# Kernel optimization log

Hardware: AMD Instinct MI355X
Metric: run time of the kernel (lower is better)

The kernel has to match this reference:

```python
import jax, jax.numpy as jnp
import numpy as np

N_NODES = 100000
N_EDGES = 1000000
N_GRAPHS = 2048
MOL_DIM = 9
HID = 64


def setup_inputs() -> dict:
    key = jax.random.key(0)
    ks = jax.random.split(key, 16)
    x = jax.random.normal(ks[0], (N_NODES, MOL_DIM), dtype=jnp.float32)
    edge_src = jax.random.randint(ks[1], (N_EDGES,), 0, N_NODES)
    edge_dst = jax.random.randint(ks[2], (N_EDGES,), 0, N_NODES)
    batch = jnp.sort(jax.random.randint(ks[3], (N_NODES,), 0, N_GRAPHS))
    def lin(k, fan_in, fan_out):
        bound = 1.0 / np.sqrt(fan_in)
        kw, kb = jax.random.split(k)
        W = jax.random.uniform(kw, (fan_in, fan_out), minval=-bound, maxval=bound, dtype=jnp.float32)
        b = jax.random.uniform(kb, (fan_out,), minval=-bound, maxval=bound, dtype=jnp.float32)
        return W, b
    W1, b1 = lin(ks[4], MOL_DIM, HID)
    W2, b2 = lin(ks[5], HID, HID)
    W3, b3 = lin(ks[6], HID, HID)
    Wp1, bp1 = lin(ks[7], 2 * HID, 64)
    Wp2, bp2 = lin(ks[8], 64, 1)
    return dict(x=x, edge_src=edge_src, edge_dst=edge_dst, batch=batch,
                W1=W1, b1=b1, W2=W2, b2=b2, W3=W3, b3=b3,
                Wp1=Wp1, bp1=bp1, Wp2=Wp2, bp2=bp2)


def gcn_conv(x, edge_src, edge_dst, W, b):
    # PyG GCNConv: add self-loops, symmetric D^-1/2 (A+I) D^-1/2 normalization.
    n = x.shape[0]
    h = x @ W  # [N, out]
    ones = jnp.ones_like(edge_dst, dtype=h.dtype)
    deg = jax.ops.segment_sum(ones, edge_dst, num_segments=n) + 1.0  # self-loop counted
    dinv = jax.lax.rsqrt(deg)
    norm = dinv[edge_src] * dinv[edge_dst]  # [E]
    msg = h[edge_src] * norm[:, None]       # gather + scale
    agg = jax.ops.segment_sum(msg, edge_dst, num_segments=n)
    agg = agg + h * (1.0 / deg)[:, None]    # self-loop contribution (norm = 1/deg)
    return agg + b


def reference(x, edge_src, edge_dst, batch, W1, b1, W2, b2, W3, b3, Wp1, bp1, Wp2, bp2):
    h = jax.nn.relu(gcn_conv(x, edge_src, edge_dst, W1, b1))
    h = jax.nn.relu(gcn_conv(h, edge_src, edge_dst, W2, b2))
    h = jax.nn.relu(gcn_conv(h, edge_src, edge_dst, W3, b3))
    # global mean / max pool by graph id
    counts = jax.ops.segment_sum(jnp.ones((h.shape[0],), h.dtype), batch, num_segments=N_GRAPHS)
    sums = jax.ops.segment_sum(h, batch, num_segments=N_GRAPHS)
    mean = sums / jnp.maximum(counts, 1.0)[:, None]
    mx = jax.ops.segment_max(h, batch, num_segments=N_GRAPHS)
    mx = jnp.where(counts[:, None] > 0, mx, 0.0)
    g = jnp.concatenate([mean, mx], axis=1)  # [G, 128]
    # predictor (dropout inactive in eval mode)
    out = jax.nn.relu(g @ Wp1 + bp1) @ Wp2 + bp2
    return out
```

## Files before the change

kernel.cpp:

```cpp
#include <hip/hip_runtime.h>

#define NN 100000
#define NE 1000000
#define NG 2048
#define NBLK 98
#define CSRCAP 1800000

__device__ __forceinline__ float rl(float v, int k) {
    return __int_as_float(__builtin_amdgcn_readlane(__float_as_int(v), k));
}
__device__ __forceinline__ int rfl(int v) { return __builtin_amdgcn_readfirstlane(v); }

#define PDEG(c) (((c) + 7) & ~7)


__global__ void k_cnt(const int* __restrict__ dst, int* __restrict__ cnt,
                      int* __restrict__ ticket,
                      const int* __restrict__ batch, int* __restrict__ pcnt) {
    int i = blockIdx.x * blockDim.x + threadIdx.x;
    if (i < NE) ticket[i] = atomicAdd(&cnt[dst[i]], 1);
    if (i < NN) atomicAdd(&pcnt[batch[i]], 1);
}

__global__ void k_scan1(const int* __restrict__ cnt, int* __restrict__ bsum,
                        const float* __restrict__ x, float* __restrict__ dinv,
                        float* __restrict__ px, float* __restrict__ p1,
                        float* __restrict__ p2) {
    int t = threadIdx.x;
    int base = blockIdx.x * 1024 + t * 4;
    int4 v = {0, 0, 0, 0};
    if (base < NN) v = *(const int4*)(cnt + base);
    int s = PDEG(v.x) + PDEG(v.y) + PDEG(v.z) + PDEG(v.w);
    #pragma unroll
    for (int off = 32; off; off >>= 1) s += __shfl_down(s, off, 64);
    __shared__ int ws[4];
    if ((t & 63) == 0) ws[t >> 6] = s;
    __syncthreads();
    if (t == 0) bsum[blockIdx.x] = ws[0] + ws[1] + ws[2] + ws[3];

    if (base < NN) {
        int c[4] = {v.x, v.y, v.z, v.w};
        #pragma unroll
        for (int j2 = 0; j2 < 4; ++j2) {
            int nd = base + j2;
            float dv = rsqrtf((float)(c[j2] + 1));
            dinv[nd] = dv;
            #pragma unroll
            for (int j = 0; j < 9; ++j) px[nd * 9 + j] = x[nd * 9 + j] * dv;
        }
    } else if (base == NN) {
        #pragma unroll
        for (int j = 0; j < 9; ++j) px[NN * 9 + j] = 0.f;
        for (int j = 0; j < 64; ++j) {
            p1[(size_t)NN * 64 + j] = 0.f;
            p2[(size_t)NN * 64 + j] = 0.f;
        }
    }
}

__global__ void k_scan2(const int* __restrict__ bsum, int* __restrict__ boff, int nb) {
    __shared__ int buf[128];
    int t = threadIdx.x;
    int v = (t < nb) ? bsum[t] : 0;
    buf[t] = v;
    __syncthreads();
    for (int off = 1; off < 128; off <<= 1) {
        int u = (t >= off) ? buf[t - off] : 0;
        __syncthreads();
        buf[t] += u;
        __syncthreads();
    }
    if (t < nb) boff[t] = buf[t] - v;
}

__global__ void k_scan3(const int* __restrict__ cnt, const int* __restrict__ boff,
                        int* __restrict__ prp, int n) {
    int t = threadIdx.x;
    int base = blockIdx.x * 1024 + t * 4;
    int4 v = {0, 0, 0, 0};
    if (base < n) v = *(const int4*)(cnt + base);
    int p0 = PDEG(v.x), p1 = PDEG(v.y), p2 = PDEG(v.z), p3 = PDEG(v.w);
    int s = p0 + p1 + p2 + p3;
    int lane = t & 63;
    int ps = s;
    #pragma unroll
    for (int off = 1; off < 64; off <<= 1) {
        int u = __shfl_up(ps, off, 64);
        if (lane >= off) ps += u;
    }
    __shared__ int ws[4];
    if (lane == 63) ws[t >> 6] = ps;
    __syncthreads();
    int w = t >> 6;
    int woff = 0;
    for (int i = 0; i < 4; ++i) woff += (i < w) ? ws[i] : 0;
    int excl = boff[blockIdx.x] + woff + ps - s;
    if (base < n) {
        prp[base] = excl;          excl += p0;
        prp[base + 1] = excl;      excl += p1;
        prp[base + 2] = excl;      excl += p2;
        prp[base + 3] = excl;      excl += p3;
        if (base + 4 == n) prp[n] = excl;
    }
}

__global__ void k_padinit(int* __restrict__ csr) {
    int i = blockIdx.x * blockDim.x + threadIdx.x;
    if (i * 4 < CSRCAP) {
        int4 v = {NN, NN, NN, NN};
        *(int4*)(csr + i * 4) = v;
    }
}

__global__ void k_fill(const int* __restrict__ src, const int* __restrict__ dst,
                       const int* __restrict__ prp, const int* __restrict__ ticket,
                       int* __restrict__ csr, int E) {
    int i = blockIdx.x * blockDim.x + threadIdx.x;
    if (i < E) csr[prp[dst[i]] + ticket[i]] = src[i];
}


template <int KD, int POOL>
__global__ __launch_bounds__(256, 8)
void k_layer(const float* __restrict__ pin, const float* __restrict__ W,
             const float* __restrict__ bias, const float* __restrict__ dinv,
             const int* __restrict__ csr, const int* __restrict__ prp,
             const int* __restrict__ batch,
             float* __restrict__ pout, float* __restrict__ psum,
             float* __restrict__ pmax) {
    __shared__ float Ws[KD * 64];
    int tid = threadIdx.x;
    for (int i = tid; i < KD * 64; i += 256) Ws[i] = W[i];
    __syncthreads();
    int f = tid & 63;
    int wv = tid >> 6;
    int n0 = (blockIdx.x * 4 + wv) * 8;
    int fi = (KD < 64) ? ((f < KD) ? f : (KD - 1)) : f;

    float q0, q1, q2, q3, q4, q5, q6, q7;

#define CHUNK(E0) { \
    int s0 = csr[(E0) + 0], s1 = csr[(E0) + 1], s2 = csr[(E0) + 2], s3 = csr[(E0) + 3]; \
    int s4 = csr[(E0) + 4], s5 = csr[(E0) + 5], s6 = csr[(E0) + 6], s7 = csr[(E0) + 7]; \
    a0 += pin[(size_t)s0 * KD + fi]; a1 += pin[(size_t)s1 * KD + fi]; \
    a2 += pin[(size_t)s2 * KD + fi]; a3 += pin[(size_t)s3 * KD + fi]; \
    a0 += pin[(size_t)s4 * KD + fi]; a1 += pin[(size_t)s5 * KD + fi]; \
    a2 += pin[(size_t)s6 * KD + fi]; a3 += pin[(size_t)s7 * KD + fi]; \
}

#define GATHER(Q, J) { \
    int nd = n0 + (J); \
    int pbeg = rfl(prp[nd]); \
    int pend = rfl(prp[nd + 1]); \
    float self = pin[(size_t)nd * KD + fi]; \
    float a0 = 0.f, a1 = 0.f, a2 = 0.f, a3 = 0.f; \
    if (pbeg != pend) { \
        CHUNK(pbeg)           \
        for (int e = pbeg + 8; e < pend; e += 8) CHUNK(e) \
    } \
    Q = (self + ((a0 + a1) + (a2 + a3))) * dinv[nd]; \
}
    GATHER(q0, 0) GATHER(q1, 1) GATHER(q2, 2) GATHER(q3, 3)
    GATHER(q4, 4) GATHER(q5, 5) GATHER(q6, 6) GATHER(q7, 7)
#undef GATHER
#undef CHUNK

    float bv = bias[f];
    float o0 = bv, o1 = bv, o2 = bv, o3 = bv, o4 = bv, o5 = bv, o6 = bv, o7 = bv;
    #pragma unroll
    for (int k = 0; k < KD; ++k) {
        float wsv = Ws[k * 64 + f];
        o0 = fmaf(rl(q0, k), wsv, o0);
        o1 = fmaf(rl(q1, k), wsv, o1);
        o2 = fmaf(rl(q2, k), wsv, o2);
        o3 = fmaf(rl(q3, k), wsv, o3);
        o4 = fmaf(rl(q4, k), wsv, o4);
        o5 = fmaf(rl(q5, k), wsv, o5);
        o6 = fmaf(rl(q6, k), wsv, o6);
        o7 = fmaf(rl(q7, k), wsv, o7);
    }

    if (POOL == 0) {
#define STORE(O, J) pout[(size_t)(n0 + (J)) * 64 + f] = fmaxf(O, 0.f) * dinv[n0 + (J)];
        STORE(o0, 0) STORE(o1, 1) STORE(o2, 2) STORE(o3, 3)
        STORE(o4, 4) STORE(o5, 5) STORE(o6, 6) STORE(o7, 7)
#undef STORE
    } else {
        int g = batch[n0];
        float sum = 0.f, mx = 0.f;
#define ACCP(O, J) { \
    float r = fmaxf(O, 0.f); \
    int gj = batch[n0 + (J)]; \
    if (gj != g) { \
        atomicAdd(&psum[g * 64 + f], sum); \
        atomicMax((int*)&pmax[g * 64 + f], __float_as_int(mx)); \
        g = gj; sum = 0.f; mx = 0.f; \
    } \
    sum += r; mx = fmaxf(mx, r); \
}
        ACCP(o0, 0) ACCP(o1, 1) ACCP(o2, 2) ACCP(o3, 3)
        ACCP(o4, 4) ACCP(o5, 5) ACCP(o6, 6) ACCP(o7, 7)
#undef ACCP
        atomicAdd(&psum[g * 64 + f], sum);
        atomicMax((int*)&pmax[g * 64 + f], __float_as_int(mx));
    }
}


__global__ void k_pred(const float* __restrict__ psum, const float* __restrict__ pmax,
                       const int* __restrict__ pcnt,
                       const float* __restrict__ Wp1, const float* __restrict__ bp1,
                       const float* __restrict__ Wp2, const float* __restrict__ bp2,
                       float* __restrict__ out, int G) {
    __shared__ float gs[4][128];
    int tid = threadIdx.x;
    int li = tid >> 6;
    int lane = tid & 63;
    int gi = blockIdx.x * 4 + li;
    if (gi < G) {
        float c = fmaxf((float)pcnt[gi], 1.0f);
        gs[li][lane] = psum[gi * 64 + lane] / c;
        gs[li][64 + lane] = pmax[gi * 64 + lane];
    }
    __syncthreads();
    if (gi >= G) return;
    float acc = bp1[lane];
    #pragma unroll
    for (int k = 0; k < 128; ++k) acc += gs[li][k] * Wp1[k * 64 + lane];
    acc = fmaxf(acc, 0.f);
    float r = acc * Wp2[lane];
    #pragma unroll
    for (int off = 32; off; off >>= 1) r += __shfl_down(r, off, 64);
    if (lane == 0) out[gi] = r + bp2[0];
}


extern "C" void kernel_launch(void* const* d_in, const int* in_sizes, int n_in,
                              void* d_out, int out_size, void* d_ws, size_t ws_size,
                              hipStream_t stream) {
    const float* x    = (const float*)d_in[0];
    const int*   esrc = (const int*)d_in[1];
    const int*   edst = (const int*)d_in[2];
    const int*   batch= (const int*)d_in[3];
    const float* W1 = (const float*)d_in[4];  const float* b1 = (const float*)d_in[5];
    const float* W2 = (const float*)d_in[6];  const float* b2 = (const float*)d_in[7];
    const float* W3 = (const float*)d_in[8];  const float* b3 = (const float*)d_in[9];
    const float* Wp1= (const float*)d_in[10]; const float* bp1= (const float*)d_in[11];
    const float* Wp2= (const float*)d_in[12]; const float* bp2= (const float*)d_in[13];
    float* out = (float*)d_out;

    char* ws = (char*)d_ws;
    int*   cnt     = (int*)  (ws + 0);
    float* psum    = (float*)(ws + 400000);
    float* pmax    = (float*)(ws + 924288);
    int*   pcnt    = (int*)  (ws + 1448576);
    const size_t ZBYTES = 1456768;
    float* dinv    = (float*)(ws + 1456768);
    int*   prp     = (int*)  (ws + 1856768);
    int*   bsum    = (int*)  (ws + 2257408);
    int*   boff    = (int*)  (ws + 2257920);
    int*   csr_pad = (int*)  (ws + 2258432);
    float* p1      = (float*)(ws + 9458432);
    float* p2      = (float*)(ws + 35058688);
    int*   ticket  = (int*)  (ws + 9458432);
    float* px      = (float*)(ws + 35058688);

    hipMemsetAsync(ws, 0, ZBYTES, stream);

    k_cnt    <<<(NE + 255) / 256, 256, 0, stream>>>(edst, cnt, ticket, batch, pcnt);
    k_scan1  <<<NBLK, 256, 0, stream>>>(cnt, bsum, x, dinv, px, p1, p2);
    k_scan2  <<<1, 128, 0, stream>>>(bsum, boff, NBLK);
    k_scan3  <<<NBLK, 256, 0, stream>>>(cnt, boff, prp, NN);
    k_padinit<<<(CSRCAP / 4 + 255) / 256, 256, 0, stream>>>(csr_pad);
    k_fill   <<<(NE + 255) / 256, 256, 0, stream>>>(esrc, edst, prp, ticket, csr_pad, NE);

    int nbl = NN / 32;
    k_layer<9, 0><<<nbl, 256, 0, stream>>>(px, W1, b1, dinv, csr_pad, prp, batch, p1, psum, pmax);
    k_layer<64, 0><<<nbl, 256, 0, stream>>>(p1, W2, b2, dinv, csr_pad, prp, batch, p2, psum, pmax);
    k_layer<64, 1><<<nbl, 256, 0, stream>>>(p2, W3, b3, dinv, csr_pad, prp, batch, p1, psum, pmax);

    k_pred <<<(NG + 3) / 4, 256, 0, stream>>>(psum, pmax, pcnt, Wp1, bp1, Wp2, bp2, out, NG);
}
```

Before: 297.6 us.

## Pad CSR rows to at least 16 and interleave first two gather chunks across nodes

Each node's padded CSR segment now holds at least 16 entries, so the first two 8-edge chunks for all eight nodes a wave handles can be issued together without bounds checks. Only the remaining tail runs per node in a loop. The aim is more memory-level parallelism in the latency-bound neighbor gather. The cost is a larger CSR buffer with more padding reads, which hit the dummy row NN, plus more registers, and occupancy is lowered to 6 waves via launch_bounds. Workspace offsets shift to fit the bigger CSR.

Result: slower. 490.8 us (+64.9%).

```diff
diff --git a/kernel.cpp b/kernel.cpp
--- a/kernel.cpp
+++ b/kernel.cpp
@@ -4,14 +4,14 @@
 #define NE 1000000
 #define NG 2048
 #define NBLK 98
-#define CSRCAP 1800000
+#define CSRCAP 2600000
 
 __device__ __forceinline__ float rl(float v, int k) {
     return __int_as_float(__builtin_amdgcn_readlane(__float_as_int(v), k));
 }
 __device__ __forceinline__ int rfl(int v) { return __builtin_amdgcn_readfirstlane(v); }
 
-#define PDEG(c) (((c) + 7) & ~7)
+#define PDEG(c) (max(16, ((c) + 7) & ~7))
 
 
 __global__ void k_cnt(const int* __restrict__ dst, int* __restrict__ cnt,
@@ -121,7 +121,7 @@
 
 
 template <int KD, int POOL>
-__global__ __launch_bounds__(256, 8)
+__global__ __launch_bounds__(256, 6)
 void k_layer(const float* __restrict__ pin, const float* __restrict__ W,
              const float* __restrict__ bias, const float* __restrict__ dinv,
              const int* __restrict__ csr, const int* __restrict__ prp,
@@ -137,32 +137,37 @@
     int n0 = (blockIdx.x * 4 + wv) * 8;
     int fi = (KD < 64) ? ((f < KD) ? f : (KD - 1)) : f;
 
-    float q0, q1, q2, q3, q4, q5, q6, q7;
-
-#define CHUNK(E0) { \
+#define CHUNK(A0, A1, E0) { \
     int s0 = csr[(E0) + 0], s1 = csr[(E0) + 1], s2 = csr[(E0) + 2], s3 = csr[(E0) + 3]; \
     int s4 = csr[(E0) + 4], s5 = csr[(E0) + 5], s6 = csr[(E0) + 6], s7 = csr[(E0) + 7]; \
-    a0 += pin[(size_t)s0 * KD + fi]; a1 += pin[(size_t)s1 * KD + fi]; \
-    a2 += pin[(size_t)s2 * KD + fi]; a3 += pin[(size_t)s3 * KD + fi]; \
-    a0 += pin[(size_t)s4 * KD + fi]; a1 += pin[(size_t)s5 * KD + fi]; \
-    a2 += pin[(size_t)s6 * KD + fi]; a3 += pin[(size_t)s7 * KD + fi]; \
-}
-
-#define GATHER(Q, J) { \
-    int nd = n0 + (J); \
-    int pbeg = rfl(prp[nd]); \
-    int pend = rfl(prp[nd + 1]); \
-    float self = pin[(size_t)nd * KD + fi]; \
-    float a0 = 0.f, a1 = 0.f, a2 = 0.f, a3 = 0.f; \
-    if (pbeg != pend) { \
-        CHUNK(pbeg)           \
-        for (int e = pbeg + 8; e < pend; e += 8) CHUNK(e) \
-    } \
-    Q = (self + ((a0 + a1) + (a2 + a3))) * dinv[nd]; \
-}
-    GATHER(q0, 0) GATHER(q1, 1) GATHER(q2, 2) GATHER(q3, 3)
-    GATHER(q4, 4) GATHER(q5, 5) GATHER(q6, 6) GATHER(q7, 7)
-#undef GATHER
+    A0 += pin[(size_t)s0 * KD + fi]; A1 += pin[(size_t)s1 * KD + fi]; \
+    A0 += pin[(size_t)s2 * KD + fi]; A1 += pin[(size_t)s3 * KD + fi]; \
+    A0 += pin[(size_t)s4 * KD + fi]; A1 += pin[(size_t)s5 * KD + fi]; \
+    A0 += pin[(size_t)s6 * KD + fi]; A1 += pin[(size_t)s7 * KD + fi]; \
+}
+
+#define BOUNDS(J) \
+    int pb##J = rfl(prp[n0 + J]); int pe##J = rfl(prp[n0 + J + 1]); \
+    float a##J##0 = pin[(size_t)(n0 + J) * KD + fi]; float a##J##1 = 0.f;
+    BOUNDS(0) BOUNDS(1) BOUNDS(2) BOUNDS(3)
+    BOUNDS(4) BOUNDS(5) BOUNDS(6) BOUNDS(7)
+#undef BOUNDS
+
+#define CH0(J) CHUNK(a##J##0, a##J##1, pb##J)
+    CH0(0) CH0(1) CH0(2) CH0(3) CH0(4) CH0(5) CH0(6) CH0(7)
+#undef CH0
+#define CH1(J) CHUNK(a##J##0, a##J##1, pb##J + 8)
+    CH1(0) CH1(1) CH1(2) CH1(3) CH1(4) CH1(5) CH1(6) CH1(7)
+#undef CH1
+
+    float q0, q1, q2, q3, q4, q5, q6, q7;
+#define TAILQ(Q, J) { \
+    for (int e = pb##J + 16; e < pe##J; e += 8) CHUNK(a##J##0, a##J##1, e) \
+    Q = (a##J##0 + a##J##1) * dinv[n0 + J]; \
+}
+    TAILQ(q0, 0) TAILQ(q1, 1) TAILQ(q2, 2) TAILQ(q3, 3)
+    TAILQ(q4, 4) TAILQ(q5, 5) TAILQ(q6, 6) TAILQ(q7, 7)
+#undef TAILQ
 #undef CHUNK
 
     float bv = bias[f];
@@ -260,10 +265,10 @@
     int*   bsum    = (int*)  (ws + 2257408);
     int*   boff    = (int*)  (ws + 2257920);
     int*   csr_pad = (int*)  (ws + 2258432);
-    float* p1      = (float*)(ws + 9458432);
-    float* p2      = (float*)(ws + 35058688);
-    int*   ticket  = (int*)  (ws + 9458432);
-    float* px      = (float*)(ws + 35058688);
+    float* p1      = (float*)(ws + 12658432);
+    float* p2      = (float*)(ws + 38258688);
+    int*   ticket  = (int*)  (ws + 12658432);
+    float* px      = (float*)(ws + 38258688);
 
     hipMemsetAsync(ws, 0, ZBYTES, stream);
 
```
